# Kernel tuning notes

Hardware: AMD Instinct MI355X
Metric: run time of the kernel (lower is better)

## Reference

```python
import jax, jax.numpy as jnp
import numpy as np

IN_C, OUT_C, NUM_VARS = 8, 8, 3
MODES1, MODES2 = 16, 16
TDIM = 256
B, H, W = 16, 256, 256
SCALE = 1.0 / (IN_C * OUT_C)


def setup_inputs() -> dict:
    key = jax.random.key(0)
    k1, k2, k3, k4, k5, k6 = jax.random.split(key, 6)
    wshape = (IN_C, OUT_C, NUM_VARS, MODES1, MODES2, TDIM)
    return {
        "t": jax.random.uniform(k1, (B, TDIM), dtype=jnp.float32),
        "x": jax.random.normal(k2, (B, IN_C, NUM_VARS, H, W), dtype=jnp.float32),
        "w1r": SCALE * jax.random.uniform(k3, wshape, dtype=jnp.float32),
        "w1i": SCALE * jax.random.uniform(k4, wshape, dtype=jnp.float32),
        "w2r": SCALE * jax.random.uniform(k5, wshape, dtype=jnp.float32),
        "w2i": SCALE * jax.random.uniform(k6, wshape, dtype=jnp.float32),
    }


def reference(t, x, w1r, w1i, w2r, w2i):
    m1, m2 = MODES1, MODES2
    b, _, v, h, w = x.shape
    wf = w // 2 + 1
    w1 = (w1r + 1j * w1i).astype(jnp.complex64)
    w2 = (w2r + 1j * w2i).astype(jnp.complex64)
    tc = t.astype(jnp.complex64)

    # FFT over last two spatial axes: [b, i, v, h, wf]
    x_ft = jnp.fft.rfft2(x)

    # time-conditioned spectral weights: [b, i, o, v, m1, m2]
    tw1 = jnp.einsum("bt,iovxyt->biovxy", tc, w1)
    tw2 = jnp.einsum("bt,iovxyt->biovxy", tc, w2)

    # complex spectral mixing on the retained low/high modes
    top = jnp.einsum("bivxy,biovxy->bovxy", x_ft[:, :, :, :m1, :m2], tw1)
    bot = jnp.einsum("bivxy,biovxy->bovxy", x_ft[:, :, :, -m1:, :m2], tw2)

    out_ft = jnp.zeros((b, OUT_C, v, h, wf), dtype=jnp.complex64)
    out_ft = out_ft.at[:, :, :, :m1, :m2].set(top)
    out_ft = out_ft.at[:, :, :, -m1:, :m2].set(bot)

    return jnp.fft.irfft2(out_ft, s=(h, w))
```

## Files before the change

kernel.cpp:

```cpp
#include <hip/hip_runtime.h>

#define BB 16
#define IC 8
#define OC 8
#define NV 3
#define M1 16
#define M2 16
#define HH 256
#define WW 256
#define NIMG_IN  (BB*IC*NV)
#define NIMG_OUT (BB*OC*NV)
#define NROWS    (IC*OC*NV*M1*M2)
#define TWO_PI 6.28318530717958647692f

__global__ __launch_bounds__(256) void k1a_rowdft(const float* __restrict__ x,
                                                  float2* __restrict__ y) {
  __shared__ float2 tbl[256];
  const int tid = threadIdx.x;
  const int img = blockIdx.x >> 1;
  const int half = blockIdx.x & 1;
  const int kbase = half ? 9 : 0;
  const int kcount = half ? 8 : 9;
  {
    float s, c;
    sincosf((float)tid * (TWO_PI / 256.0f), &s, &c);
    tbl[tid] = make_float2(c, s);
  }
  __syncthreads();

  const float* xp = x + (size_t)img * 65536 + tid;
  float yr[9], yi[9];
#pragma unroll
  for (int k = 0; k < 9; k++) { yr[k] = 0.0f; yi[k] = 0.0f; }

  int mb = 0;
#pragma unroll 4
  for (int h = 0; h < 256; h++) {
    float xv = xp[h * 256];
    int m = mb;
#pragma unroll
    for (int k = 0; k < 9; k++) {
      float2 e = tbl[m];
      yr[k] = fmaf(e.x, xv, yr[k]);
      yi[k] = fmaf(-e.y, xv, yi[k]);
      m = (m + h) & 255;
    }
    mb = (mb + kbase) & 255;
  }
  float2* yo = y + (size_t)img * 4352 + (size_t)kbase * 256 + tid;
  for (int k = 0; k < kcount; k++) yo[k * 256] = make_float2(yr[k], yi[k]);
}

__global__ __launch_bounds__(256) void k1b_coldft(const float2* __restrict__ y,
                                                  float2* __restrict__ Xf) {
  __shared__ float2 tbl[256];
  __shared__ float2 yb[17 * 257];
  const int tid = threadIdx.x;
  const int img = blockIdx.x;
  {
    float s, c;
    sincosf((float)tid * (TWO_PI / 256.0f), &s, &c);
    tbl[tid] = make_float2(c, s);
  }
  const float2* yg = y + (size_t)img * 4352;
  for (int n = tid; n < 4352; n += 256) {
    int kx = n >> 8, w = n & 255;
    yb[kx * 257 + w] = yg[n];
  }
  __syncthreads();

  float2* XfImg = Xf + (size_t)img * 512;
  for (int n = tid; n < 512; n += 256) {
    int row = n >> 4, ky = n & 15;
    int kxl = (row < 16) ? row : (32 - row);
    float sgn = (row < 16) ? 1.0f : -1.0f;
    float Xr = 0.0f, Xi = 0.0f;
    int m = 0;
    for (int w2 = 0; w2 < 256; w2++) {
      float2 yv = yb[kxl * 257 + w2];
      float2 e = tbl[m];
      m = (m + ky) & 255;
      float yy = yv.y * sgn;
      Xr += yv.x * e.x + yy * e.y;
      Xi += yy * e.x - yv.x * e.y;
    }
    XfImg[n] = make_float2(Xr, Xi);
  }
}

__global__ __launch_bounds__(256) void k2_tw(const float* __restrict__ t,
                                             const float* __restrict__ w1r,
                                             const float* __restrict__ w1i,
                                             const float* __restrict__ w2r,
                                             const float* __restrict__ w2i,
                                             float2* __restrict__ tw1,
                                             float2* __restrict__ tw2) {
  __shared__ float tL[16 * 257];
  const int tid = threadIdx.x;
  for (int n = tid; n < 16 * 256; n += 256) {
    int b = n >> 8, tt = n & 255;
    tL[b * 257 + tt] = t[b * 256 + tt];
  }
  __syncthreads();

  const int lane = tid & 63;
  const int wv = tid >> 6;
  const int b = lane & 15;
  const int rl = lane >> 4;
  const int row = (blockIdx.x * 4 + wv) * 4 + rl;

  const float4* p1r = (const float4*)(w1r + (size_t)row * 256);
  const float4* p1i = (const float4*)(w1i + (size_t)row * 256);
  const float4* p2r = (const float4*)(w2r + (size_t)row * 256);
  const float4* p2i = (const float4*)(w2i + (size_t)row * 256);
  const float* tb = tL + b * 257;

  float a1r = 0.0f, a1i = 0.0f, a2r = 0.0f, a2i = 0.0f;
  for (int ti = 0; ti < 64; ti++) {
    float4 v1r = p1r[ti];
    float4 v1i = p1i[ti];
    float4 v2r = p2r[ti];
    float4 v2i = p2i[ti];
    float t0 = tb[4 * ti + 0];
    float t1 = tb[4 * ti + 1];
    float t2 = tb[4 * ti + 2];
    float t3 = tb[4 * ti + 3];
    a1r += t0 * v1r.x + t1 * v1r.y + t2 * v1r.z + t3 * v1r.w;
    a1i += t0 * v1i.x + t1 * v1i.y + t2 * v1i.z + t3 * v1i.w;
    a2r += t0 * v2r.x + t1 * v2r.y + t2 * v2r.z + t3 * v2r.w;
    a2i += t0 * v2i.x + t1 * v2i.y + t2 * v2i.z + t3 * v2i.w;
  }
  tw1[(size_t)b * NROWS + row] = make_float2(a1r, a1i);
  tw2[(size_t)b * NROWS + row] = make_float2(a2r, a2i);
}

__global__ __launch_bounds__(256) void k3_mix(const float2* __restrict__ Xf,
                                              const float2* __restrict__ tw1,
                                              const float2* __restrict__ tw2,
                                              float2* __restrict__ ftT,
                                              float2* __restrict__ ftB) {
  const int n = blockIdx.x * 256 + threadIdx.x;
  const int xy = n & 255;
  const int ov = n >> 8;
  const int v = ov % 3;
  const int o = (ov / 3) & 7;
  const int b = n / (OC * NV * 256);

  float tr = 0.0f, ti2 = 0.0f, br = 0.0f, bi = 0.0f;
#pragma unroll
  for (int i = 0; i < IC; i++) {
    const float2 xt = Xf[(size_t)(((b * IC + i) * NV + v) << 9) + xy];
    const float2 xb = Xf[(size_t)(((b * IC + i) * NV + v) << 9) + 256 + xy];
    const int r = ((i * OC + o) * NV + v) * 256 + xy;
    float2 u1 = tw1[(size_t)b * NROWS + r];
    float2 u2 = tw2[(size_t)b * NROWS + r];
    tr += xt.x * u1.x - xt.y * u1.y;
    ti2 += xt.x * u1.y + xt.y * u1.x;
    br += xb.x * u2.x - xb.y * u2.y;
    bi += xb.x * u2.y + xb.y * u2.x;
  }
  const int nout = ((b * OC + o) * NV + v) * 256 + xy;
  ftT[nout] = make_float2(tr, ti2);
  ftB[nout] = make_float2(br, bi);
}

__global__ __launch_bounds__(256) void k4a_hdft(const float2* __restrict__ ftT,
                                                const float2* __restrict__ ftB,
                                                float2* __restrict__ G) {
  __shared__ float2 tbl[256];
  __shared__ float2 ftL[512];
  const int tid = threadIdx.x;
  const int img = blockIdx.x;
  {
    float s, c;
    sincosf((float)tid * (TWO_PI / 256.0f), &s, &c);
    tbl[tid] = make_float2(c, s);
    ftL[tid] = ftT[(size_t)img * 256 + tid];
    ftL[256 + tid] = ftB[(size_t)img * 256 + tid];
  }
  __syncthreads();

  const int h = tid;
  float gr[16], gi[16];
#pragma unroll
  for (int ky = 0; ky < 16; ky++) { gr[ky] = 0.0f; gi[ky] = 0.0f; }
  for (int row = 0; row < 32; row++) {
    int kxv = (row < 16) ? row : (224 + row);
    float2 e = tbl[(kxv * h) & 255];
#pragma unroll
    for (int ky = 0; ky < 16; ky++) {
      float2 f = ftL[row * 16 + ky];
      gr[ky] += f.x * e.x - f.y * e.y;
      gi[ky] += f.x * e.y + f.y * e.x;
    }
  }
  float2* Gi = G + (size_t)img * 4096;
#pragma unroll
  for (int ky = 0; ky < 16; ky++) Gi[ky * 256 + h] = make_float2(gr[ky], gi[ky]);
}

__global__ __launch_bounds__(256) void k4b_wdft(const float2* __restrict__ G,
                                                float* __restrict__ out) {
  __shared__ float2 tbl[256];
  __shared__ float2 PL[16 * 256];
  __shared__ float2 gt[512];
  const int tid = threadIdx.x;
  const int img = blockIdx.x >> 3;
  const int h0 = (blockIdx.x & 7) * 32;
  {
    float s, c;
    sincosf((float)tid * (TWO_PI / 256.0f), &s, &c);
    tbl[tid] = make_float2(c, s);
  }
  __syncthreads();
  for (int n = tid; n < 4096; n += 256) {
    int ky = n >> 8, w = n & 255;
    float2 e = tbl[(ky * w) & 255];
    float sc = (ky == 0) ? (1.0f / 65536.0f) : (2.0f / 65536.0f);
    PL[n] = make_float2(e.x * sc, e.y * sc);
  }
  const float2* Gi = G + (size_t)img * 4096;
  for (int n = tid; n < 512; n += 256) {
    int ky = n >> 5, hh = n & 31;
    gt[n] = Gi[ky * 256 + h0 + hh];
  }
  __syncthreads();

  const int w0 = tid & 63;
  const int hq = tid >> 6;
  float acc[8][4];
#pragma unroll
  for (int a = 0; a < 8; a++)
#pragma unroll
    for (int j = 0; j < 4; j++) acc[a][j] = 0.0f;

#pragma unroll 4
  for (int ky = 0; ky < 16; ky++) {
    float2 p0 = PL[ky * 256 + w0];
    float2 p1 = PL[ky * 256 + w0 + 64];
    float2 p2 = PL[ky * 256 + w0 + 128];
    float2 p3 = PL[ky * 256 + w0 + 192];
#pragma unroll
    for (int a = 0; a < 8; a++) {
      float2 g = gt[ky * 32 + hq * 8 + a];
      acc[a][0] += g.x * p0.x - g.y * p0.y;
      acc[a][1] += g.x * p1.x - g.y * p1.y;
      acc[a][2] += g.x * p2.x - g.y * p2.y;
      acc[a][3] += g.x * p3.x - g.y * p3.y;
    }
  }
  float* obase = out + (size_t)img * 65536 + (size_t)(h0 + hq * 8) * 256;
#pragma unroll
  for (int a = 0; a < 8; a++) {
#pragma unroll
    for (int j = 0; j < 4; j++) obase[a * 256 + w0 + 64 * j] = acc[a][j];
  }
}

extern "C" void kernel_launch(void* const* d_in, const int* in_sizes, int n_in,
                              void* d_out, int out_size, void* d_ws, size_t ws_size,
                              hipStream_t stream) {
  const float* t = (const float*)d_in[0];
  const float* x = (const float*)d_in[1];
  const float* w1r = (const float*)d_in[2];
  const float* w1i = (const float*)d_in[3];
  const float* w2r = (const float*)d_in[4];
  const float* w2i = (const float*)d_in[5];
  float* out = (float*)d_out;

  float2* R1 = (float2*)d_ws;
  float2* y = R1;
  float2* tw1 = R1;
  float2* tw2 = R1 + 786432;
  float2* G = R1;
  float2* Xf = R1 + 1671168;
  float2* ftT = Xf + 196608;
  float2* ftB = ftT + 98304;

  k1a_rowdft<<<NIMG_IN * 2, 256, 0, stream>>>(x, y);
  k1b_coldft<<<NIMG_IN, 256, 0, stream>>>(y, Xf);
  k2_tw<<<NROWS / 16, 256, 0, stream>>>(t, w1r, w1i, w2r, w2i, tw1, tw2);
  k3_mix<<<(BB * OC * NV * 256) / 256, 256, 0, stream>>>(Xf, tw1, tw2, ftT, ftB);
  k4a_hdft<<<NIMG_OUT, 256, 0, stream>>>(ftT, ftB, G);
  k4b_wdft<<<NIMG_OUT * 8, 256, 0, stream>>>(G, out);
}
```

Baseline: 513.9 us.

## Vectorize row DFT with split-H reduction and tile weight contraction through LDS

The row DFT kernel now has each thread handle four adjacent columns via float4 loads. The H dimension is split across four thread groups, and their partial sums are combined through a two-step shared-memory reduction. This reuses each twiddle lookup for four columns and raises memory-level parallelism, at the cost of more registers and extra barriers. The time-weight kernel now stages 16 weight rows into swizzled LDS, so each weight row is read from global memory once and reused across all 16 batch entries instead of being re-fetched per batch lane.

```diff
diff --git a/kernel.cpp b/kernel.cpp
--- a/kernel.cpp
+++ b/kernel.cpp
@@ -13,9 +13,10 @@
 #define NROWS    (IC*OC*NV*M1*M2)
 #define TWO_PI 6.28318530717958647692f
 
-__global__ __launch_bounds__(256) void k1a_rowdft(const float* __restrict__ x,
-                                                  float2* __restrict__ y) {
+__global__ __launch_bounds__(256, 4) void k1a_rowdft(const float* __restrict__ x,
+                                                     float2* __restrict__ y) {
   __shared__ float2 tbl[256];
+  __shared__ float red[2][64][73];
   const int tid = threadIdx.x;
   const int img = blockIdx.x >> 1;
   const int half = blockIdx.x & 1;
@@ -28,27 +29,71 @@
   }
   __syncthreads();
 
-  const float* xp = x + (size_t)img * 65536 + tid;
-  float yr[9], yi[9];
-#pragma unroll
-  for (int k = 0; k < 9; k++) { yr[k] = 0.0f; yi[k] = 0.0f; }
-
-  int mb = 0;
-#pragma unroll 4
-  for (int h = 0; h < 256; h++) {
-    float xv = xp[h * 256];
-    int m = mb;
-#pragma unroll
-    for (int k = 0; k < 9; k++) {
+  const int col4 = tid & 63;
+  const int hq = tid >> 6;
+  const float4* xp = (const float4*)(x + (size_t)img * 65536) + col4;
+
+  float ar[9][4], ai[9][4];
+#pragma unroll
+  for (int j = 0; j < 9; j++)
+#pragma unroll
+    for (int c = 0; c < 4; c++) { ar[j][c] = 0.0f; ai[j][c] = 0.0f; }
+
+  for (int hi = 0; hi < 64; hi++) {
+    const int h = hq * 64 + hi;
+    float4 xv = xp[(size_t)h * 64];
+    int m = (kbase * h) & 255;
+#pragma unroll
+    for (int j = 0; j < 9; j++) {
       float2 e = tbl[m];
-      yr[k] = fmaf(e.x, xv, yr[k]);
-      yi[k] = fmaf(-e.y, xv, yi[k]);
       m = (m + h) & 255;
-    }
-    mb = (mb + kbase) & 255;
-  }
-  float2* yo = y + (size_t)img * 4352 + (size_t)kbase * 256 + tid;
-  for (int k = 0; k < kcount; k++) yo[k * 256] = make_float2(yr[k], yi[k]);
+      ar[j][0] = fmaf(e.x, xv.x, ar[j][0]);
+      ai[j][0] = fmaf(-e.y, xv.x, ai[j][0]);
+      ar[j][1] = fmaf(e.x, xv.y, ar[j][1]);
+      ai[j][1] = fmaf(-e.y, xv.y, ai[j][1]);
+      ar[j][2] = fmaf(e.x, xv.z, ar[j][2]);
+      ai[j][2] = fmaf(-e.y, xv.z, ai[j][2]);
+      ar[j][3] = fmaf(e.x, xv.w, ar[j][3]);
+      ai[j][3] = fmaf(-e.y, xv.w, ai[j][3]);
+    }
+  }
+
+  if (hq >= 2) {
+    float* p = red[hq - 2][col4];
+#pragma unroll
+    for (int j = 0; j < 9; j++)
+#pragma unroll
+      for (int c = 0; c < 4; c++) { p[j * 8 + c * 2] = ar[j][c]; p[j * 8 + c * 2 + 1] = ai[j][c]; }
+  }
+  __syncthreads();
+  if (hq < 2) {
+    const float* p = red[hq][col4];
+#pragma unroll
+    for (int j = 0; j < 9; j++)
+#pragma unroll
+      for (int c = 0; c < 4; c++) { ar[j][c] += p[j * 8 + c * 2]; ai[j][c] += p[j * 8 + c * 2 + 1]; }
+  }
+  __syncthreads();
+  if (hq == 1) {
+    float* p = red[0][col4];
+#pragma unroll
+    for (int j = 0; j < 9; j++)
+#pragma unroll
+      for (int c = 0; c < 4; c++) { p[j * 8 + c * 2] = ar[j][c]; p[j * 8 + c * 2 + 1] = ai[j][c]; }
+  }
+  __syncthreads();
+  if (hq == 0) {
+    const float* p = red[0][col4];
+    float2* yo = y + (size_t)img * 4352;
+    for (int j = 0; j < kcount; j++) {
+#pragma unroll
+      for (int c = 0; c < 4; c++) {
+        float rr = ar[j][c] + p[j * 8 + c * 2];
+        float ii = ai[j][c] + p[j * 8 + c * 2 + 1];
+        yo[(kbase + j) * 256 + col4 * 4 + c] = make_float2(rr, ii);
+      }
+    }
+  }
 }
 
 __global__ __launch_bounds__(256) void k1b_coldft(const float2* __restrict__ y,
@@ -95,43 +140,54 @@
                                              const float* __restrict__ w2i,
                                              float2* __restrict__ tw1,
                                              float2* __restrict__ tw2) {
-  __shared__ float tL[16 * 257];
-  const int tid = threadIdx.x;
-  for (int n = tid; n < 16 * 256; n += 256) {
-    int b = n >> 8, tt = n & 255;
-    tL[b * 257 + tt] = t[b * 256 + tt];
-  }
-  __syncthreads();
-
-  const int lane = tid & 63;
-  const int wv = tid >> 6;
-  const int b = lane & 15;
-  const int rl = lane >> 4;
-  const int row = (blockIdx.x * 4 + wv) * 4 + rl;
-
-  const float4* p1r = (const float4*)(w1r + (size_t)row * 256);
-  const float4* p1i = (const float4*)(w1i + (size_t)row * 256);
-  const float4* p2r = (const float4*)(w2r + (size_t)row * 256);
-  const float4* p2i = (const float4*)(w2i + (size_t)row * 256);
-  const float* tb = tL + b * 257;
-
-  float a1r = 0.0f, a1i = 0.0f, a2r = 0.0f, a2i = 0.0f;
-  for (int ti = 0; ti < 64; ti++) {
-    float4 v1r = p1r[ti];
-    float4 v1i = p1i[ti];
-    float4 v2r = p2r[ti];
-    float4 v2i = p2i[ti];
-    float t0 = tb[4 * ti + 0];
-    float t1 = tb[4 * ti + 1];
-    float t2 = tb[4 * ti + 2];
-    float t3 = tb[4 * ti + 3];
-    a1r += t0 * v1r.x + t1 * v1r.y + t2 * v1r.z + t3 * v1r.w;
-    a1i += t0 * v1i.x + t1 * v1i.y + t2 * v1i.z + t3 * v1i.w;
-    a2r += t0 * v2r.x + t1 * v2r.y + t2 * v2r.z + t3 * v2r.w;
-    a2i += t0 * v2i.x + t1 * v2i.y + t2 * v2i.z + t3 * v2i.w;
-  }
-  tw1[(size_t)b * NROWS + row] = make_float2(a1r, a1i);
-  tw2[(size_t)b * NROWS + row] = make_float2(a2r, a2i);
+  __shared__ float tL[16 * 260];
+  __shared__ float4 wA[2][16 * 64];
+  const int tid = threadIdx.x;
+  const int row0 = blockIdx.x * 16;
+  const int b = tid >> 4;
+  const int r = tid & 15;
+  const int c = r & 7;
+
+  {
+    const float4* tg = (const float4*)t;
+    float4* ts = (float4*)tL;
+    for (int n = tid; n < 1024; n += 256) ts[(n >> 6) * 65 + (n & 63)] = tg[n];
+  }
+
+  float o1r, o1i, o2r, o2i;
+  const float4* tb4 = (const float4*)tL + b * 65;
+
+  for (int pass = 0; pass < 2; pass++) {
+    const float* wa = pass ? w2r : w1r;
+    const float* wb = pass ? w2i : w1i;
+    const float4* ga = (const float4*)(wa + (size_t)row0 * 256);
+    const float4* gb = (const float4*)(wb + (size_t)row0 * 256);
+    for (int n = tid; n < 1024; n += 256) {
+      int rr = n >> 6, t4 = n & 63;
+      int sidx = (rr << 6) | (t4 ^ (rr & 7));
+      wA[0][sidx] = ga[n];
+      wA[1][sidx] = gb[n];
+    }
+    __syncthreads();
+
+    const float4* ra4 = wA[0] + (r << 6);
+    const float4* rb4 = wA[1] + (r << 6);
+    float arr = 0.0f, aii = 0.0f;
+#pragma unroll 8
+    for (int t4 = 0; t4 < 64; t4++) {
+      float4 tv = tb4[t4];
+      int s = t4 ^ c;
+      float4 va = ra4[s];
+      float4 vb = rb4[s];
+      arr += tv.x * va.x + tv.y * va.y + tv.z * va.z + tv.w * va.w;
+      aii += tv.x * vb.x + tv.y * vb.y + tv.z * vb.z + tv.w * vb.w;
+    }
+    if (pass) { o2r = arr; o2i = aii; } else { o1r = arr; o1i = aii; }
+    __syncthreads();
+  }
+
+  tw1[(size_t)b * NROWS + row0 + r] = make_float2(o1r, o1i);
+  tw2[(size_t)b * NROWS + row0 + r] = make_float2(o2r, o2i);
 }
 
 __global__ __launch_bounds__(256) void k3_mix(const float2* __restrict__ Xf,
```

After: 467.9 us. 1.1x faster.
